# Kernel tuning notes

Hardware: AMD Instinct MI355X
Metric: run time of the kernel (lower is better)

The kernel has to match this reference:

```python
import jax, jax.numpy as jnp
import numpy as np

DIM = 2048
DIM_HEAD = 128
HEADS = 16
BATCH = 1
SEQ = 2048
EPS = 1e-5
MASK_VALUE = 1e-10  # faithful to original module (not -inf)
SCALE = DIM_HEAD ** -0.5


def setup_inputs() -> dict:
    key = jax.random.key(0)
    ks = jax.random.split(key, 7)
    x = jax.random.normal(ks[0], (BATCH, SEQ, DIM), dtype=jnp.float32)
    pos_bias = jax.random.normal(ks[1], (HEADS, SEQ, SEQ), dtype=jnp.float32)
    gamma = jnp.ones((DIM,), dtype=jnp.float32)
    wq = jax.random.normal(ks[2], (DIM, HEADS * DIM_HEAD), dtype=jnp.float32)
    wk = jax.random.normal(ks[3], (DIM, DIM_HEAD), dtype=jnp.float32)
    wv = jax.random.normal(ks[4], (DIM, DIM_HEAD), dtype=jnp.float32)
    wo = jax.random.normal(ks[5], (HEADS * DIM_HEAD, DIM), dtype=jnp.float32)
    # causal mask [SEQ, SEQ]
    mask = jnp.tril(jnp.ones((SEQ, SEQ), dtype=jnp.bool_))
    return {"x": x, "pos_bias": pos_bias, "gamma": gamma,
            "wq": wq, "wk": wk, "wv": wv, "wo": wo, "mask": mask}


def reference(x, pos_bias, gamma, wq, wk, wv, wo, mask):
    # RMSNorm
    inv_norm = jax.lax.rsqrt(jnp.mean(jnp.square(x), axis=-1, keepdims=True) + EPS)
    xn = inv_norm * x * gamma
    # projections (multi-query: single shared K/V head)
    q = xn @ wq                                  # [b, n, h*d]
    k = xn @ wk                                  # [b, n, d]
    v = xn @ wv                                  # [b, n, d]
    b, n, _ = q.shape
    q = q.reshape(b, n, HEADS, DIM_HEAD).transpose(0, 2, 1, 3)  # [b, h, n, d]
    q = q * SCALE
    sim = jnp.einsum('bhid,bjd->bhij', q, k)     # [b, h, i, j]
    sim = sim + pos_bias                          # pos_bias [h, n, n] broadcasts
    sim = jnp.where(mask, sim, MASK_VALUE)
    attn = jax.nn.softmax(sim, axis=-1)
    out = jnp.einsum('bhij,bjd->bhid', attn, v)  # [b, h, n, d]
    out = out.transpose(0, 2, 1, 3).reshape(b, n, HEADS * DIM_HEAD)
    return out @ wo
```

## Files before the change

### kernel.cpp

```cpp
#include <hip/hip_runtime.h>
#include <math.h>

#define SEQ 2048
#define DIM 2048
#define NH 16
#define DH 128
#define NKV 2304
#define KOFF 2048
#define VOFF 2176
#define QK_SCALE 0.08838834764831845f

typedef _Float16 f16;
typedef _Float16 f16x8 __attribute__((ext_vector_type(8)));
typedef _Float16 f16x4 __attribute__((ext_vector_type(4)));
typedef float f32x4 __attribute__((ext_vector_type(4)));

__device__ __forceinline__ void gload16(const f16* g, f16* l) {
    __builtin_amdgcn_global_load_lds(
        (const __attribute__((address_space(1))) void*)g,
        (__attribute__((address_space(3))) void*)l,
        16, 0, 0);
}

__global__ __launch_bounds__(256) void rmsnorm_split_k(
    const float* __restrict__ x, const float* __restrict__ gamma,
    f16* __restrict__ oh, f16* __restrict__ ol)
{
    int row = blockIdx.x, tid = threadIdx.x;
    const float4* xr = (const float4*)(x + (size_t)row * DIM);
    float4 a0 = xr[tid], a1 = xr[tid + 256];
    float ss = a0.x*a0.x + a0.y*a0.y + a0.z*a0.z + a0.w*a0.w
             + a1.x*a1.x + a1.y*a1.y + a1.z*a1.z + a1.w*a1.w;
    #pragma unroll
    for (int off = 1; off < 64; off <<= 1) ss += __shfl_xor(ss, off, 64);
    __shared__ float red[4];
    if ((tid & 63) == 0) red[tid >> 6] = ss;
    __syncthreads();
    float inv = 1.0f / sqrtf((red[0] + red[1] + red[2] + red[3]) * (1.0f / DIM) + 1e-5f);
    const float4* gr = (const float4*)gamma;
    float4 g0 = gr[tid], g1 = gr[tid + 256];
    float v[8] = { a0.x*inv*g0.x, a0.y*inv*g0.y, a0.z*inv*g0.z, a0.w*inv*g0.w,
                   a1.x*inv*g1.x, a1.y*inv*g1.y, a1.z*inv*g1.z, a1.w*inv*g1.w };
    f16x4 h0, l0, h1, l1;
    #pragma unroll
    for (int i = 0; i < 4; i++) {
        f16 h = (f16)v[i];   h0[i] = h; l0[i] = (f16)(v[i]   - (float)h);
        f16 g = (f16)v[i+4]; h1[i] = g; l1[i] = (f16)(v[i+4] - (float)g);
    }
    size_t base = (size_t)row * DIM + tid * 4;
    *(f16x4*)&oh[base] = h0;  *(f16x4*)&oh[base + 1024] = h1;
    *(f16x4*)&ol[base] = l0;  *(f16x4*)&ol[base + 1024] = l1;
}

template<bool WLO>
__global__ __launch_bounds__(256) void transpose_split_k(
    const float* __restrict__ in, f16* __restrict__ oh, f16* __restrict__ ol,
    int ldin, int outld)
{
    __shared__ float t[32][33];
    int tx = threadIdx.x, ty = threadIdx.y;
    int c0 = blockIdx.x * 32, r0 = blockIdx.y * 32;
    #pragma unroll
    for (int yy = 0; yy < 4; yy++)
        t[ty + yy*8][tx] = in[(size_t)(r0 + ty + yy*8) * ldin + c0 + tx];
    __syncthreads();
    #pragma unroll
    for (int yy = 0; yy < 4; yy++) {
        float v = t[tx][ty + yy*8];
        size_t o = (size_t)(c0 + ty + yy*8) * outld + r0 + tx;
        f16 h = (f16)v; oh[o] = h;
        if (WLO) ol[o] = (f16)(v - (float)h);
    }
}

__global__ __launch_bounds__(256) void transpose_f16_k(
    const f16* __restrict__ in, f16* __restrict__ out, int ldin, int outld)
{
    __shared__ f16 t[32][33];
    int tx = threadIdx.x, ty = threadIdx.y;
    int c0 = blockIdx.x * 32, r0 = blockIdx.y * 32;
    #pragma unroll
    for (int yy = 0; yy < 4; yy++)
        t[ty + yy*8][tx] = in[(size_t)(r0 + ty + yy*8) * ldin + c0 + tx];
    __syncthreads();
    #pragma unroll
    for (int yy = 0; yy < 4; yy++)
        out[(size_t)(c0 + ty + yy*8) * outld + r0 + tx] = t[tx][ty + yy*8];
}

__global__ __launch_bounds__(64) void vsuf_k(
    const f16* __restrict__ Vt, float* __restrict__ Vsuf)
{
    int d = blockIdx.x;
    int lane = threadIdx.x;
    float vals[32]; float s = 0.f;
    const f16* row = Vt + (size_t)d * SEQ + lane * 32;
    #pragma unroll
    for (int u = 0; u < 32; u++) { vals[u] = (float)row[u]; s += vals[u]; }
    float acc = s;
    #pragma unroll
    for (int off = 1; off < 64; off <<= 1) {
        float other = __shfl_down(acc, off, 64);
        if (lane + off < 64) acc += other;
    }
    float run = acc - s;
    for (int u = 31; u >= 0; u--) {
        Vsuf[(size_t)(lane * 32 + u) * DH + d] = run;
        run += vals[u];
    }
}

template<int PASSES, int OUTMODE>
__global__ __launch_bounds__(256) void gemm_k(
    const f16* __restrict__ Ah, const f16* __restrict__ Al,
    const f16* __restrict__ Bh, const f16* __restrict__ Bl,
    float* __restrict__ C, f16* __restrict__ Ch, f16* __restrict__ Cl,
    int N, int K, float scale, int scale_cols)
{
    __shared__ f16 sa_h[128 * 32];
    __shared__ f16 sb_h[128 * 32];
    __shared__ f16 sa_l[PASSES == 3 ? 128 * 32 : 8];
    __shared__ f16 sb_l[PASSES == 3 ? 128 * 32 : 8];
    int tid = threadIdx.x;
    int wave = tid >> 6, lane = tid & 63, quad = lane >> 4, l16 = lane & 15;
    int m0 = blockIdx.x * 128, n0 = blockIdx.y * 128;
    int wm = (wave & 1) * 64, wn = (wave >> 1) * 64;
    f32x4 acc[4][4] = {};

    int r0s = wave * 16 + (lane >> 2);
    int cs  = (lane & 3) * 8;
    const f16* gA0 = Ah + (size_t)(m0 + r0s) * K + cs;
    const f16* gA1 = Ah + (size_t)(m0 + r0s + 64) * K + cs;
    const f16* gB0 = Bh + (size_t)(n0 + r0s) * K + cs;
    const f16* gB1 = Bh + (size_t)(n0 + r0s + 64) * K + cs;
    const f16* hA0 = Al + (size_t)(m0 + r0s) * K + cs;
    const f16* hA1 = Al + (size_t)(m0 + r0s + 64) * K + cs;
    const f16* hB0 = Bl + (size_t)(n0 + r0s) * K + cs;
    const f16* hB1 = Bl + (size_t)(n0 + r0s + 64) * K + cs;
    f16* lA0 = &sa_h[(size_t)r0s * 32 + cs];
    f16* lA1 = &sa_h[(size_t)(r0s + 64) * 32 + cs];
    f16* lB0 = &sb_h[(size_t)r0s * 32 + cs];
    f16* lB1 = &sb_h[(size_t)(r0s + 64) * 32 + cs];
    f16* mA0 = &sa_l[(size_t)r0s * 32 + cs];
    f16* mA1 = &sa_l[(size_t)(r0s + 64) * 32 + cs];
    f16* mB0 = &sb_l[(size_t)r0s * 32 + cs];
    f16* mB1 = &sb_l[(size_t)(r0s + 64) * 32 + cs];

    for (int k0 = 0; k0 < K; k0 += 32) {
        __syncthreads();
        gload16(gA0 + k0, lA0);
        gload16(gA1 + k0, lA1);
        gload16(gB0 + k0, lB0);
        gload16(gB1 + k0, lB1);
        if constexpr (PASSES == 3) {
            gload16(hA0 + k0, mA0);
            gload16(hA1 + k0, mA1);
            gload16(hB0 + k0, mB0);
            gload16(hB1 + k0, mB1);
        }
        __syncthreads();
        f16x8 ah[4], bh[4], al[4], bl[4];
        #pragma unroll
        for (int t = 0; t < 4; t++) {
            ah[t] = *(const f16x8*)&sa_h[(wm + t*16 + l16) * 32 + quad * 8];
            bh[t] = *(const f16x8*)&sb_h[(wn + t*16 + l16) * 32 + quad * 8];
        }
        if constexpr (PASSES == 3) {
            #pragma unroll
            for (int t = 0; t < 4; t++) {
                al[t] = *(const f16x8*)&sa_l[(wm + t*16 + l16) * 32 + quad * 8];
                bl[t] = *(const f16x8*)&sb_l[(wn + t*16 + l16) * 32 + quad * 8];
            }
        }
        #pragma unroll
        for (int i = 0; i < 4; i++)
            #pragma unroll
            for (int j = 0; j < 4; j++) {
                acc[i][j] = __builtin_amdgcn_mfma_f32_16x16x32_f16(ah[i], bh[j], acc[i][j], 0, 0, 0);
                if constexpr (PASSES == 3) {
                    acc[i][j] = __builtin_amdgcn_mfma_f32_16x16x32_f16(ah[i], bl[j], acc[i][j], 0, 0, 0);
                    acc[i][j] = __builtin_amdgcn_mfma_f32_16x16x32_f16(al[i], bh[j], acc[i][j], 0, 0, 0);
                }
            }
    }
    #pragma unroll
    for (int i = 0; i < 4; i++)
        #pragma unroll
        for (int j = 0; j < 4; j++) {
            int row = m0 + wm + i*16 + quad*4;
            int col = n0 + wn + j*16 + l16;
            float s = (col < scale_cols) ? scale : 1.0f;
            #pragma unroll
            for (int r = 0; r < 4; r++) {
                float v = acc[i][j][r] * s;
                if constexpr (OUTMODE == 0) {
                    C[(size_t)(row + r) * N + col] = v;
                } else {
                    f16 h = (f16)v;
                    Ch[(size_t)(row + r) * N + col] = h;
                    Cl[(size_t)(row + r) * N + col] = (f16)(v - (float)h);
                }
            }
        }
}

__global__ __launch_bounds__(256) void attn_k(
    const f16* __restrict__ Ph, const f16* __restrict__ Pl,
    const f16* __restrict__ Vt, const float* __restrict__ bias,
    const float* __restrict__ Vsuf, f16* __restrict__ Out)
{
    __shared__ f16 skh[64][136];
    __shared__ f16 skl[64][136];
    __shared__ f16 sv[128][72];
    __shared__ f16 sp[4][16][72];
    int tid = threadIdx.x, wave = tid >> 6, lane = tid & 63;
    int quad = lane >> 4, l16 = lane & 15;
    int h = blockIdx.y;
    int i0 = ((int)gridDim.x - 1 - (int)blockIdx.x) * 64;
    int qrow = i0 + wave * 16 + l16;

    f16x8 qh[4], ql[4];
    #pragma unroll
    for (int kt = 0; kt < 4; kt++) {
        size_t off = (size_t)qrow * NKV + h * DH + kt * 32 + quad * 8;
        qh[kt] = *(const f16x8*)(Ph + off);
        ql[kt] = *(const f16x8*)(Pl + off);
    }
    f32x4 o[8];
    f32x4 zero = {0.f, 0.f, 0.f, 0.f};
    #pragma unroll
    for (int dt = 0; dt < 8; dt++) o[dt] = zero;
    float mrun[4], lrun[4];
    #pragma unroll
    for (int r = 0; r < 4; r++) { mrun[r] = -1e30f; lrun[r] = 0.f; }

    int krow = tid >> 2, kc4 = tid & 3;
    int vd = tid >> 1, vcg = tid & 1;
    const float* brow = bias + (size_t)h * SEQ * SEQ;
    int ibase = i0 + wave * 16 + quad * 4;

    int ntile = i0 / 64 + 1;
    for (int jt = 0; jt < ntile; jt++) {
        int j0 = jt * 64;
        __syncthreads();
        #pragma unroll
        for (int cc = 0; cc < 4; cc++) {
            int ch = kc4 + cc * 4;
            size_t goff = (size_t)(j0 + krow) * NKV + KOFF + ch * 8;
            *(f16x8*)&skh[krow][ch * 8] = *(const f16x8*)(Ph + goff);
            *(f16x8*)&skl[krow][ch * 8] = *(const f16x8*)(Pl + goff);
        }
        #pragma unroll
        for (int cc = 0; cc < 4; cc++) {
            int ch = vcg + cc * 2;
            *(f16x8*)&sv[vd][ch * 8] = *(const f16x8*)(Vt + (size_t)vd * SEQ + j0 + ch * 8);
        }
        __syncthreads();

        f32x4 s[4];
        #pragma unroll
        for (int nt = 0; nt < 4; nt++) s[nt] = zero;
        #pragma unroll
        for (int nt = 0; nt < 4; nt++)
            #pragma unroll
            for (int kt = 0; kt < 4; kt++) {
                f16x8 kh = *(const f16x8*)&skh[nt*16 + l16][kt*32 + quad*8];
                f16x8 kl = *(const f16x8*)&skl[nt*16 + l16][kt*32 + quad*8];
                s[nt] = __builtin_amdgcn_mfma_f32_16x16x32_f16(qh[kt], kh, s[nt], 0, 0, 0);
                s[nt] = __builtin_amdgcn_mfma_f32_16x16x32_f16(qh[kt], kl, s[nt], 0, 0, 0);
                s[nt] = __builtin_amdgcn_mfma_f32_16x16x32_f16(ql[kt], kh, s[nt], 0, 0, 0);
            }
        #pragma unroll
        for (int nt = 0; nt < 4; nt++) {
            int jg = j0 + nt*16 + l16;
            #pragma unroll
            for (int r = 0; r < 4; r++) {
                int ig = ibase + r;
                float v = s[nt][r] + brow[(size_t)ig * SEQ + jg];
                s[nt][r] = (jg <= ig) ? v : 1e-10f;
            }
        }
        #pragma unroll
        for (int r = 0; r < 4; r++) {
            float mx = fmaxf(fmaxf(s[0][r], s[1][r]), fmaxf(s[2][r], s[3][r]));
            mx = fmaxf(mx, __shfl_xor(mx, 1, 64));
            mx = fmaxf(mx, __shfl_xor(mx, 2, 64));
            mx = fmaxf(mx, __shfl_xor(mx, 4, 64));
            mx = fmaxf(mx, __shfl_xor(mx, 8, 64));
            float mn = fmaxf(mrun[r], mx);
            float alpha = __expf(mrun[r] - mn);
            mrun[r] = mn;
            float rs = 0.f;
            #pragma unroll
            for (int nt = 0; nt < 4; nt++) {
                float p = __expf(s[nt][r] - mn);
                s[nt][r] = p; rs += p;
            }
            rs += __shfl_xor(rs, 1, 64);
            rs += __shfl_xor(rs, 2, 64);
            rs += __shfl_xor(rs, 4, 64);
            rs += __shfl_xor(rs, 8, 64);
            lrun[r] = lrun[r] * alpha + rs;
            #pragma unroll
            for (int dt = 0; dt < 8; dt++) o[dt][r] *= alpha;
            #pragma unroll
            for (int nt = 0; nt < 4; nt++)
                sp[wave][quad*4 + r][nt*16 + l16] = (f16)s[nt][r];
        }
        #pragma unroll
        for (int ks = 0; ks < 2; ks++) {
            f16x8 pa = *(const f16x8*)&sp[wave][l16][ks*32 + quad*8];
            #pragma unroll
            for (int dt = 0; dt < 8; dt++) {
                f16x8 vb = *(const f16x8*)&sv[dt*16 + l16][ks*32 + quad*8];
                o[dt] = __builtin_amdgcn_mfma_f32_16x16x32_f16(pa, vb, o[dt], 0, 0, 0);
            }
        }
    }
    #pragma unroll
    for (int dt = 0; dt < 8; dt++) {
        int col = h * DH + dt*16 + l16;
        #pragma unroll
        for (int r = 0; r < 4; r++) {
            int ig = i0 + wave*16 + quad*4 + r;
            int nmask = SEQ - 1 - ig;
            float mfin = fmaxf(mrun[r], 1e-10f);
            float al = __expf(mrun[r] - mfin);
            float pm = (nmask > 0) ? __expf(1e-10f - mfin) : 0.f;
            float lfin = lrun[r] * al + (float)nmask * pm;
            float num = o[dt][r] * al + pm * Vsuf[(size_t)ig * DH + dt*16 + l16];
            Out[(size_t)ig * DIM + col] = (f16)(num / lfin);
        }
    }
}

extern "C" void kernel_launch(void* const* d_in, const int* in_sizes, int n_in,
                              void* d_out, int out_size, void* d_ws, size_t ws_size,
                              hipStream_t stream)
{
    const float* x     = (const float*)d_in[0];
    const float* bias  = (const float*)d_in[1];
    const float* gamma = (const float*)d_in[2];
    const float* wq    = (const float*)d_in[3];
    const float* wk    = (const float*)d_in[4];
    const float* wv    = (const float*)d_in[5];
    const float* wo    = (const float*)d_in[6];
    float* out = (float*)d_out;
    char* ws = (char*)d_ws;

    const size_t MB = 1024 * 1024;
    f16* xn_h   = (f16*)(ws);
    f16* xn_l   = (f16*)(ws + 8  * MB);
    f16* wT_h   = (f16*)(ws + 16 * MB);
    f16* wT_l   = (f16*)(ws + 25 * MB);
    f16* woT_h  = (f16*)(ws + 34 * MB);
    f16* proj_h = (f16*)(ws + 42 * MB);
    f16* proj_l = (f16*)(ws + 51 * MB);
    float* vsuf = (float*)(ws + 60 * MB);
    f16* attn_o = xn_h;
    f16* vT     = xn_l;

    dim3 tb(32, 8);

    rmsnorm_split_k<<<SEQ, 256, 0, stream>>>(x, gamma, xn_h, xn_l);

    transpose_split_k<true><<<dim3(64, 64), tb, 0, stream>>>(wq, wT_h, wT_l, DIM, DIM);
    transpose_split_k<true><<<dim3(4, 64),  tb, 0, stream>>>(wk, wT_h + (size_t)KOFF * DIM,
                                                             wT_l + (size_t)KOFF * DIM, DH, DIM);
    transpose_split_k<true><<<dim3(4, 64),  tb, 0, stream>>>(wv, wT_h + (size_t)VOFF * DIM,
                                                             wT_l + (size_t)VOFF * DIM, DH, DIM);
    transpose_split_k<false><<<dim3(64, 64), tb, 0, stream>>>(wo, woT_h, nullptr, DIM, DIM);

    gemm_k<3, 1><<<dim3(16, 18), 256, 0, stream>>>(xn_h, xn_l, wT_h, wT_l,
                                                   nullptr, proj_h, proj_l,
                                                   NKV, DIM, QK_SCALE, DIM);

    transpose_f16_k<<<dim3(4, 64), tb, 0, stream>>>(proj_h + VOFF, vT, NKV, SEQ);
    vsuf_k<<<DH, 64, 0, stream>>>(vT, vsuf);

    attn_k<<<dim3(32, 16), 256, 0, stream>>>(proj_h, proj_l, vT, bias, vsuf, attn_o);

    gemm_k<1, 0><<<dim3(16, 16), 256, 0, stream>>>(attn_o, attn_o, woT_h, woT_h,
                                                   out, nullptr, nullptr,
                                                   DIM, DIM, 1.0f, 0);
}
```

Baseline: 783.1 us.

## Split causal attention rows into KV halves with atomic work queue and merge

The attention kernel becomes persistent: each block pulls work units from an atomic counter, longest-first. Each query-row tile of 64 rows is split into two halves of its causal KV range. The partial outputs, row max and row sum are written to a workspace buffer, and a separate merge kernel combines them with the masked-suffix correction. The aim is to balance the triangular causal workload across CUs. The cost is partial writes, an extra merge launch, a counter-reset launch, and rounding the normalized partials to fp16.

Result: faster. 680.1 us (-13.2%).

```diff
diff --git a/kernel.cpp b/kernel.cpp
--- a/kernel.cpp
+++ b/kernel.cpp
@@ -9,6 +9,9 @@
 #define KOFF 2048
 #define VOFF 2176
 #define QK_SCALE 0.08838834764831845f
+
+#define NUNITS 1008
+#define RECS 16896
 
 typedef _Float16 f16;
 typedef _Float16 f16x8 __attribute__((ext_vector_type(8)));
@@ -109,6 +112,8 @@
         run += vals[u];
     }
 }
+
+__global__ void init_counter_k(int* c) { c[0] = 0; }
 
 template<int PASSES, int OUTMODE>
 __global__ __launch_bounds__(256) void gemm_k(
@@ -207,130 +212,217 @@
 __global__ __launch_bounds__(256) void attn_k(
     const f16* __restrict__ Ph, const f16* __restrict__ Pl,
     const f16* __restrict__ Vt, const float* __restrict__ bias,
-    const float* __restrict__ Vsuf, f16* __restrict__ Out)
+    const float* __restrict__ Vsuf, f16* __restrict__ Out,
+    char* __restrict__ partial, int* __restrict__ counter)
 {
     __shared__ f16 skh[64][136];
     __shared__ f16 skl[64][136];
     __shared__ f16 sv[128][72];
     __shared__ f16 sp[4][16][72];
+    __shared__ int s_unit;
     int tid = threadIdx.x, wave = tid >> 6, lane = tid & 63;
     int quad = lane >> 4, l16 = lane & 15;
-    int h = blockIdx.y;
-    int i0 = ((int)gridDim.x - 1 - (int)blockIdx.x) * 64;
-    int qrow = i0 + wave * 16 + l16;
-
-    f16x8 qh[4], ql[4];
-    #pragma unroll
-    for (int kt = 0; kt < 4; kt++) {
-        size_t off = (size_t)qrow * NKV + h * DH + kt * 32 + quad * 8;
-        qh[kt] = *(const f16x8*)(Ph + off);
-        ql[kt] = *(const f16x8*)(Pl + off);
-    }
-    f32x4 o[8];
-    f32x4 zero = {0.f, 0.f, 0.f, 0.f};
-    #pragma unroll
-    for (int dt = 0; dt < 8; dt++) o[dt] = zero;
-    float mrun[4], lrun[4];
-    #pragma unroll
-    for (int r = 0; r < 4; r++) { mrun[r] = -1e30f; lrun[r] = 0.f; }
-
     int krow = tid >> 2, kc4 = tid & 3;
     int vd = tid >> 1, vcg = tid & 1;
-    const float* brow = bias + (size_t)h * SEQ * SEQ;
-    int ibase = i0 + wave * 16 + quad * 4;
-
-    int ntile = i0 / 64 + 1;
-    for (int jt = 0; jt < ntile; jt++) {
-        int j0 = jt * 64;
+    f32x4 zero = {0.f, 0.f, 0.f, 0.f};
+
+    for (;;) {
         __syncthreads();
-        #pragma unroll
-        for (int cc = 0; cc < 4; cc++) {
-            int ch = kc4 + cc * 4;
-            size_t goff = (size_t)(j0 + krow) * NKV + KOFF + ch * 8;
-            *(f16x8*)&skh[krow][ch * 8] = *(const f16x8*)(Ph + goff);
-            *(f16x8*)&skl[krow][ch * 8] = *(const f16x8*)(Pl + goff);
-        }
-        #pragma unroll
-        for (int cc = 0; cc < 4; cc++) {
-            int ch = vcg + cc * 2;
-            *(f16x8*)&sv[vd][ch * 8] = *(const f16x8*)(Vt + (size_t)vd * SEQ + j0 + ch * 8);
-        }
+        if (tid == 0) s_unit = atomicAdd(counter, 1);
         __syncthreads();
-
-        f32x4 s[4];
-        #pragma unroll
-        for (int nt = 0; nt < 4; nt++) s[nt] = zero;
-        #pragma unroll
-        for (int nt = 0; nt < 4; nt++)
-            #pragma unroll
-            for (int kt = 0; kt < 4; kt++) {
-                f16x8 kh = *(const f16x8*)&skh[nt*16 + l16][kt*32 + quad*8];
-                f16x8 kl = *(const f16x8*)&skl[nt*16 + l16][kt*32 + quad*8];
-                s[nt] = __builtin_amdgcn_mfma_f32_16x16x32_f16(qh[kt], kh, s[nt], 0, 0, 0);
-                s[nt] = __builtin_amdgcn_mfma_f32_16x16x32_f16(qh[kt], kl, s[nt], 0, 0, 0);
-                s[nt] = __builtin_amdgcn_mfma_f32_16x16x32_f16(ql[kt], kh, s[nt], 0, 0, 0);
-            }
-        #pragma unroll
-        for (int nt = 0; nt < 4; nt++) {
-            int jg = j0 + nt*16 + l16;
+        int u = s_unit;
+        if (u >= NUNITS) break;
+
+        int a, h, jt_begin, jt_end, is_half;
+        if (u < 992) {
+            int pr = u >> 5; a = 31 - pr; h = u & 15;
+            int half = (u >> 4) & 1;
+            int ntt = a + 1, nth = (ntt + 1) >> 1;
+            jt_begin = half ? nth : 0;
+            jt_end   = half ? ntt : nth;
+            is_half = 1;
+        } else {
+            a = 0; h = u - 992; jt_begin = 0; jt_end = 1; is_half = 0;
+        }
+        int i0 = a * 64;
+        int qrow = i0 + wave * 16 + l16;
+        int ibase = i0 + wave * 16 + quad * 4;
+        const float* brow = bias + (size_t)h * SEQ * SEQ;
+
+        f16x8 qh[4], ql[4];
+        #pragma unroll
+        for (int kt = 0; kt < 4; kt++) {
+            size_t off = (size_t)qrow * NKV + h * DH + kt * 32 + quad * 8;
+            qh[kt] = *(const f16x8*)(Ph + off);
+            ql[kt] = *(const f16x8*)(Pl + off);
+        }
+        f32x4 o[8];
+        #pragma unroll
+        for (int dt = 0; dt < 8; dt++) o[dt] = zero;
+        float mrun[4], lrun[4];
+        #pragma unroll
+        for (int r = 0; r < 4; r++) { mrun[r] = -1e30f; lrun[r] = 0.f; }
+
+        for (int jt = jt_begin; jt < jt_end; jt++) {
+            int j0 = jt * 64;
+            __syncthreads();
+            #pragma unroll
+            for (int cc = 0; cc < 4; cc++) {
+                int ch = kc4 + cc * 4;
+                size_t goff = (size_t)(j0 + krow) * NKV + KOFF + ch * 8;
+                *(f16x8*)&skh[krow][ch * 8] = *(const f16x8*)(Ph + goff);
+                *(f16x8*)&skl[krow][ch * 8] = *(const f16x8*)(Pl + goff);
+            }
+            #pragma unroll
+            for (int cc = 0; cc < 4; cc++) {
+                int ch = vcg + cc * 2;
+                *(f16x8*)&sv[vd][ch * 8] = *(const f16x8*)(Vt + (size_t)vd * SEQ + j0 + ch * 8);
+            }
+            __syncthreads();
+
+            f32x4 s[4];
+            #pragma unroll
+            for (int nt = 0; nt < 4; nt++) s[nt] = zero;
+            #pragma unroll
+            for (int nt = 0; nt < 4; nt++)
+                #pragma unroll
+                for (int kt = 0; kt < 4; kt++) {
+                    f16x8 kh = *(const f16x8*)&skh[nt*16 + l16][kt*32 + quad*8];
+                    f16x8 kl = *(const f16x8*)&skl[nt*16 + l16][kt*32 + quad*8];
+                    s[nt] = __builtin_amdgcn_mfma_f32_16x16x32_f16(qh[kt], kh, s[nt], 0, 0, 0);
+                    s[nt] = __builtin_amdgcn_mfma_f32_16x16x32_f16(qh[kt], kl, s[nt], 0, 0, 0);
+                    s[nt] = __builtin_amdgcn_mfma_f32_16x16x32_f16(ql[kt], kh, s[nt], 0, 0, 0);
+                }
+            #pragma unroll
+            for (int nt = 0; nt < 4; nt++) {
+                int jg = j0 + nt*16 + l16;
+                #pragma unroll
+                for (int r = 0; r < 4; r++) {
+                    int ig = ibase + r;
+                    float v = s[nt][r] + brow[(size_t)ig * SEQ + jg];
+                    s[nt][r] = (jg <= ig) ? v : 1e-10f;
+                }
+            }
             #pragma unroll
             for (int r = 0; r < 4; r++) {
-                int ig = ibase + r;
-                float v = s[nt][r] + brow[(size_t)ig * SEQ + jg];
-                s[nt][r] = (jg <= ig) ? v : 1e-10f;
-            }
-        }
-        #pragma unroll
-        for (int r = 0; r < 4; r++) {
-            float mx = fmaxf(fmaxf(s[0][r], s[1][r]), fmaxf(s[2][r], s[3][r]));
-            mx = fmaxf(mx, __shfl_xor(mx, 1, 64));
-            mx = fmaxf(mx, __shfl_xor(mx, 2, 64));
-            mx = fmaxf(mx, __shfl_xor(mx, 4, 64));
-            mx = fmaxf(mx, __shfl_xor(mx, 8, 64));
-            float mn = fmaxf(mrun[r], mx);
-            float alpha = __expf(mrun[r] - mn);
-            mrun[r] = mn;
-            float rs = 0.f;
-            #pragma unroll
-            for (int nt = 0; nt < 4; nt++) {
-                float p = __expf(s[nt][r] - mn);
-                s[nt][r] = p; rs += p;
-            }
-            rs += __shfl_xor(rs, 1, 64);
-            rs += __shfl_xor(rs, 2, 64);
-            rs += __shfl_xor(rs, 4, 64);
-            rs += __shfl_xor(rs, 8, 64);
-            lrun[r] = lrun[r] * alpha + rs;
-            #pragma unroll
-            for (int dt = 0; dt < 8; dt++) o[dt][r] *= alpha;
-            #pragma unroll
-            for (int nt = 0; nt < 4; nt++)
-                sp[wave][quad*4 + r][nt*16 + l16] = (f16)s[nt][r];
-        }
-        #pragma unroll
-        for (int ks = 0; ks < 2; ks++) {
-            f16x8 pa = *(const f16x8*)&sp[wave][l16][ks*32 + quad*8];
+                float mx = fmaxf(fmaxf(s[0][r], s[1][r]), fmaxf(s[2][r], s[3][r]));
+                mx = fmaxf(mx, __shfl_xor(mx, 1, 64));
+                mx = fmaxf(mx, __shfl_xor(mx, 2, 64));
+                mx = fmaxf(mx, __shfl_xor(mx, 4, 64));
+                mx = fmaxf(mx, __shfl_xor(mx, 8, 64));
+                float mn = fmaxf(mrun[r], mx);
+                float alpha = __expf(mrun[r] - mn);
+                mrun[r] = mn;
+                float rs = 0.f;
+                #pragma unroll
+                for (int nt = 0; nt < 4; nt++) {
+                    float p = __expf(s[nt][r] - mn);
+                    s[nt][r] = p; rs += p;
+                }
+                rs += __shfl_xor(rs, 1, 64);
+                rs += __shfl_xor(rs, 2, 64);
+                rs += __shfl_xor(rs, 4, 64);
+                rs += __shfl_xor(rs, 8, 64);
+                lrun[r] = lrun[r] * alpha + rs;
+                #pragma unroll
+                for (int dt = 0; dt < 8; dt++) o[dt][r] *= alpha;
+                #pragma unroll
+                for (int nt = 0; nt < 4; nt++)
+                    sp[wave][quad*4 + r][nt*16 + l16] = (f16)s[nt][r];
+            }
+            #pragma unroll
+            for (int ks = 0; ks < 2; ks++) {
+                f16x8 pa = *(const f16x8*)&sp[wave][l16][ks*32 + quad*8];
+                #pragma unroll
+                for (int dt = 0; dt < 8; dt++) {
+                    f16x8 vb = *(const f16x8*)&sv[dt*16 + l16][ks*32 + quad*8];
+                    o[dt] = __builtin_amdgcn_mfma_f32_16x16x32_f16(pa, vb, o[dt], 0, 0, 0);
+                }
+            }
+        }
+
+        if (is_half) {
+            char* rec = partial + (size_t)u * RECS;
+            f16*   on = (f16*)rec;
+            float* pm = (float*)(rec + 16384);
+            float* pl = (float*)(rec + 16640);
+            float invl[4];
+            #pragma unroll
+            for (int r = 0; r < 4; r++) invl[r] = 1.0f / lrun[r];
+            #pragma unroll
+            for (int dt = 0; dt < 8; dt++)
+                #pragma unroll
+                for (int r = 0; r < 4; r++)
+                    on[(wave*16 + quad*4 + r) * DH + dt*16 + l16] = (f16)(o[dt][r] * invl[r]);
+            if (l16 == 0) {
+                #pragma unroll
+                for (int r = 0; r < 4; r++) {
+                    int row = wave*16 + quad*4 + r;
+                    pm[row] = mrun[r]; pl[row] = lrun[r];
+                }
+            }
+        } else {
             #pragma unroll
             for (int dt = 0; dt < 8; dt++) {
-                f16x8 vb = *(const f16x8*)&sv[dt*16 + l16][ks*32 + quad*8];
-                o[dt] = __builtin_amdgcn_mfma_f32_16x16x32_f16(pa, vb, o[dt], 0, 0, 0);
-            }
-        }
-    }
-    #pragma unroll
-    for (int dt = 0; dt < 8; dt++) {
-        int col = h * DH + dt*16 + l16;
-        #pragma unroll
-        for (int r = 0; r < 4; r++) {
-            int ig = i0 + wave*16 + quad*4 + r;
-            int nmask = SEQ - 1 - ig;
-            float mfin = fmaxf(mrun[r], 1e-10f);
-            float al = __expf(mrun[r] - mfin);
-            float pm = (nmask > 0) ? __expf(1e-10f - mfin) : 0.f;
-            float lfin = lrun[r] * al + (float)nmask * pm;
-            float num = o[dt][r] * al + pm * Vsuf[(size_t)ig * DH + dt*16 + l16];
-            Out[(size_t)ig * DIM + col] = (f16)(num / lfin);
-        }
+                int col = h * DH + dt*16 + l16;
+                #pragma unroll
+                for (int r = 0; r < 4; r++) {
+                    int ig = i0 + wave*16 + quad*4 + r;
+                    int nmask = SEQ - 1 - ig;
+                    float mfin = fmaxf(mrun[r], 1e-10f);
+                    float al = __expf(mrun[r] - mfin);
+                    float pmv = (nmask > 0) ? __expf(1e-10f - mfin) : 0.f;
+                    float lfin = lrun[r] * al + (float)nmask * pmv;
+                    float num = o[dt][r] * al + pmv * Vsuf[(size_t)ig * DH + dt*16 + l16];
+                    Out[(size_t)ig * DIM + col] = (f16)(num / lfin);
+                }
+            }
+        }
+    }
+}
+
+__global__ __launch_bounds__(256) void attn_merge_k(
+    const char* __restrict__ partial, const float* __restrict__ Vsuf,
+    f16* __restrict__ Out)
+{
+    int b = blockIdx.x;
+    int pr = b >> 4, h = b & 15;
+    int a = 31 - pr, i0 = a * 64;
+    int u0 = pr * 32 + h, u1 = u0 + 16;
+    const char* r0 = partial + (size_t)u0 * RECS;
+    const char* r1 = partial + (size_t)u1 * RECS;
+    const f16*   o1p = (const f16*)r0;
+    const float* m1p = (const float*)(r0 + 16384);
+    const float* l1p = (const float*)(r0 + 16640);
+    const f16*   o2p = (const f16*)r1;
+    const float* m2p = (const float*)(r1 + 16384);
+    const float* l2p = (const float*)(r1 + 16640);
+    int t = threadIdx.x;
+    int col = (t & 15) * 8;
+    int rg = t >> 4;
+    #pragma unroll
+    for (int rr = 0; rr < 4; rr++) {
+        int row = rg * 4 + rr, ig = i0 + row;
+        float m1 = m1p[row], l1 = l1p[row], m2 = m2p[row], l2 = l2p[row];
+        float m = fmaxf(m1, m2);
+        float w1 = __expf(m1 - m) * l1;
+        float w2 = __expf(m2 - m) * l2;
+        float l = w1 + w2;
+        int nmask = SEQ - 1 - ig;
+        float mf = fmaxf(m, 1e-10f);
+        float al = __expf(m - mf);
+        float pm = (nmask > 0) ? __expf(1e-10f - mf) : 0.f;
+        float lf = l * al + (float)nmask * pm;
+        f16x8 o1 = *(const f16x8*)&o1p[row * DH + col];
+        f16x8 o2 = *(const f16x8*)&o2p[row * DH + col];
+        const float* vs = &Vsuf[(size_t)ig * DH + col];
+        f16x8 outv;
+        #pragma unroll
+        for (int e = 0; e < 8; e++) {
+            float num = ((float)o1[e] * w1 + (float)o2[e] * w2) * al + pm * vs[e];
+            outv[e] = (f16)(num / lf);
+        }
+        *(f16x8*)&Out[(size_t)ig * DIM + h * DH + col] = outv;
     }
 }
 
@@ -357,6 +449,8 @@
     f16* proj_h = (f16*)(ws + 42 * MB);
     f16* proj_l = (f16*)(ws + 51 * MB);
     float* vsuf = (float*)(ws + 60 * MB);
+    char* partial = ws + 16 * MB;
+    int* counter  = (int*)(ws + 33 * MB);
     f16* attn_o = xn_h;
     f16* vT     = xn_l;
 
@@ -377,8 +471,11 @@
 
     transpose_f16_k<<<dim3(4, 64), tb, 0, stream>>>(proj_h + VOFF, vT, NKV, SEQ);
     vsuf_k<<<DH, 64, 0, stream>>>(vT, vsuf);
-
-    attn_k<<<dim3(32, 16), 256, 0, stream>>>(proj_h, proj_l, vT, bias, vsuf, attn_o);
+    init_counter_k<<<1, 1, 0, stream>>>(counter);
+
+    attn_k<<<512, 256, 0, stream>>>(proj_h, proj_l, vT, bias, vsuf, attn_o,
+                                    partial, counter);
+    attn_merge_k<<<496, 256, 0, stream>>>(partial, vsuf, attn_o);
 
     gemm_k<1, 0><<<dim3(16, 16), 256, 0, stream>>>(attn_o, attn_o, woT_h, woT_h,
                                                    out, nullptr, nullptr,
```

## Split-KV persistent attention with atomic work queue, async bias prefetch, and merge pass

Applied to the files above, without the earlier changes.

Replaces the per-block causal attention kernel with a persistent kernel that pulls work units from an atomic counter. Each unit is one 16-row query group and head, with long rows split into up to four KV chunks so that work is balanced across the causal triangle. Each wave reads K and V straight from global memory, prefetches pos_bias into double-buffered LDS using global_load_lds with an XOR swizzle, and writes normalized partial outputs plus max and sum statistics. A separate merge kernel then combines the partials and adds the masked-suffix correction, which now uses a per-64-column-chunk V sum table. This adds a counter reset launch, a merge launch and partial-buffer traffic, and drops the LDS reuse of K/V across waves.

Measured after the change: 741.2 us. -5.4%, faster.

```diff
diff --git a/kernel.cpp b/kernel.cpp
--- a/kernel.cpp
+++ b/kernel.cpp
@@ -10,12 +10,22 @@
 #define VOFF 2176
 #define QK_SCALE 0.08838834764831845f
 
+#define NUNITS2 5120
+#define RECB 4224
+#define RECPH 288
+
 typedef _Float16 f16;
 typedef _Float16 f16x8 __attribute__((ext_vector_type(8)));
 typedef _Float16 f16x4 __attribute__((ext_vector_type(4)));
 typedef float f32x4 __attribute__((ext_vector_type(4)));
 
 __device__ __forceinline__ void gload16(const f16* g, f16* l) {
+    __builtin_amdgcn_global_load_lds(
+        (const __attribute__((address_space(1))) void*)g,
+        (__attribute__((address_space(3))) void*)l,
+        16, 0, 0);
+}
+__device__ __forceinline__ void gload16f(const float* g, float* l) {
     __builtin_amdgcn_global_load_lds(
         (const __attribute__((address_space(1))) void*)g,
         (__attribute__((address_space(3))) void*)l,
@@ -88,27 +98,25 @@
         out[(size_t)(c0 + ty + yy*8) * outld + r0 + tx] = t[tx][ty + yy*8];
 }
 
-__global__ __launch_bounds__(64) void vsuf_k(
-    const f16* __restrict__ Vt, float* __restrict__ Vsuf)
-{
-    int d = blockIdx.x;
-    int lane = threadIdx.x;
-    float vals[32]; float s = 0.f;
-    const f16* row = Vt + (size_t)d * SEQ + lane * 32;
-    #pragma unroll
-    for (int u = 0; u < 32; u++) { vals[u] = (float)row[u]; s += vals[u]; }
-    float acc = s;
+__global__ __launch_bounds__(64) void vsuft_k(
+    const f16* __restrict__ Vt, float* __restrict__ Vsuft)
+{
+    int d = blockIdx.x, t = threadIdx.x;
+    float s = 0.f;
+    if (t < 32) {
+        const f16* row = Vt + (size_t)d * SEQ + t * 64;
+        #pragma unroll
+        for (int u = 0; u < 64; u++) s += (float)row[u];
+    }
     #pragma unroll
     for (int off = 1; off < 64; off <<= 1) {
-        float other = __shfl_down(acc, off, 64);
-        if (lane + off < 64) acc += other;
-    }
-    float run = acc - s;
-    for (int u = 31; u >= 0; u--) {
-        Vsuf[(size_t)(lane * 32 + u) * DH + d] = run;
-        run += vals[u];
-    }
-}
+        float v = __shfl_down(s, off, 64);
+        s += (t + off < 64) ? v : 0.f;
+    }
+    if (t <= 32) Vsuft[t * DH + d] = (t < 32) ? s : 0.f;
+}
+
+__global__ void init_counter_k(int* c) { c[0] = 0; }
 
 template<int PASSES, int OUTMODE>
 __global__ __launch_bounds__(256) void gemm_k(
@@ -204,133 +212,230 @@
         }
 }
 
-__global__ __launch_bounds__(256) void attn_k(
+__global__ __launch_bounds__(256) void attn2_k(
     const f16* __restrict__ Ph, const f16* __restrict__ Pl,
     const f16* __restrict__ Vt, const float* __restrict__ bias,
-    const float* __restrict__ Vsuf, f16* __restrict__ Out)
-{
-    __shared__ f16 skh[64][136];
-    __shared__ f16 skl[64][136];
-    __shared__ f16 sv[128][72];
-    __shared__ f16 sp[4][16][72];
+    const float* __restrict__ Vsuft, f16* __restrict__ Out,
+    char* __restrict__ partial, int* __restrict__ counter)
+{
+    __shared__ float sbias[4 * 2 * 1024];
+    __shared__ f16 sp[4 * 16 * 72];
     int tid = threadIdx.x, wave = tid >> 6, lane = tid & 63;
     int quad = lane >> 4, l16 = lane & 15;
-    int h = blockIdx.y;
-    int i0 = ((int)gridDim.x - 1 - (int)blockIdx.x) * 64;
-    int qrow = i0 + wave * 16 + l16;
-
-    f16x8 qh[4], ql[4];
-    #pragma unroll
-    for (int kt = 0; kt < 4; kt++) {
-        size_t off = (size_t)qrow * NKV + h * DH + kt * 32 + quad * 8;
-        qh[kt] = *(const f16x8*)(Ph + off);
-        ql[kt] = *(const f16x8*)(Pl + off);
-    }
-    f32x4 o[8];
+    float* mybias = &sbias[wave * 2048];
+    f16* mysp = &sp[wave * 1152];
+    int dma_r = lane >> 4;
+    int dma_c = lane & 15;
     f32x4 zero = {0.f, 0.f, 0.f, 0.f};
-    #pragma unroll
-    for (int dt = 0; dt < 8; dt++) o[dt] = zero;
-    float mrun[4], lrun[4];
-    #pragma unroll
-    for (int r = 0; r < 4; r++) { mrun[r] = -1e30f; lrun[r] = 0.f; }
-
-    int krow = tid >> 2, kc4 = tid & 3;
-    int vd = tid >> 1, vcg = tid & 1;
-    const float* brow = bias + (size_t)h * SEQ * SEQ;
-    int ibase = i0 + wave * 16 + quad * 4;
-
-    int ntile = i0 / 64 + 1;
-    for (int jt = 0; jt < ntile; jt++) {
-        int j0 = jt * 64;
-        __syncthreads();
-        #pragma unroll
-        for (int cc = 0; cc < 4; cc++) {
-            int ch = kc4 + cc * 4;
-            size_t goff = (size_t)(j0 + krow) * NKV + KOFF + ch * 8;
-            *(f16x8*)&skh[krow][ch * 8] = *(const f16x8*)(Ph + goff);
-            *(f16x8*)&skl[krow][ch * 8] = *(const f16x8*)(Pl + goff);
-        }
-        #pragma unroll
-        for (int cc = 0; cc < 4; cc++) {
-            int ch = vcg + cc * 2;
-            *(f16x8*)&sv[vd][ch * 8] = *(const f16x8*)(Vt + (size_t)vd * SEQ + j0 + ch * 8);
-        }
-        __syncthreads();
-
-        f32x4 s[4];
-        #pragma unroll
-        for (int nt = 0; nt < 4; nt++) s[nt] = zero;
-        #pragma unroll
-        for (int nt = 0; nt < 4; nt++)
-            #pragma unroll
-            for (int kt = 0; kt < 4; kt++) {
-                f16x8 kh = *(const f16x8*)&skh[nt*16 + l16][kt*32 + quad*8];
-                f16x8 kl = *(const f16x8*)&skl[nt*16 + l16][kt*32 + quad*8];
-                s[nt] = __builtin_amdgcn_mfma_f32_16x16x32_f16(qh[kt], kh, s[nt], 0, 0, 0);
-                s[nt] = __builtin_amdgcn_mfma_f32_16x16x32_f16(qh[kt], kl, s[nt], 0, 0, 0);
-                s[nt] = __builtin_amdgcn_mfma_f32_16x16x32_f16(ql[kt], kh, s[nt], 0, 0, 0);
-            }
-        #pragma unroll
-        for (int nt = 0; nt < 4; nt++) {
-            int jg = j0 + nt*16 + l16;
-            #pragma unroll
-            for (int r = 0; r < 4; r++) {
-                int ig = ibase + r;
-                float v = s[nt][r] + brow[(size_t)ig * SEQ + jg];
-                s[nt][r] = (jg <= ig) ? v : 1e-10f;
-            }
-        }
-        #pragma unroll
-        for (int r = 0; r < 4; r++) {
-            float mx = fmaxf(fmaxf(s[0][r], s[1][r]), fmaxf(s[2][r], s[3][r]));
-            mx = fmaxf(mx, __shfl_xor(mx, 1, 64));
-            mx = fmaxf(mx, __shfl_xor(mx, 2, 64));
-            mx = fmaxf(mx, __shfl_xor(mx, 4, 64));
-            mx = fmaxf(mx, __shfl_xor(mx, 8, 64));
-            float mn = fmaxf(mrun[r], mx);
-            float alpha = __expf(mrun[r] - mn);
-            mrun[r] = mn;
+
+    for (;;) {
+        int u0;
+        if (lane == 0) u0 = atomicAdd(counter, 1);
+        int u = __shfl(u0, 0, 64);
+        if (u >= NUNITS2) break;
+
+        int h = u & 15, t = u >> 4;
+        int g, chunk, n;
+        if (t < 128)      { g = 127 - (t >> 2); chunk = t & 3; n = 4; }
+        else if (t < 224) { int s5 = t - 128; int q5 = s5 / 3; g = 95 - q5; chunk = s5 - q5 * 3; n = 3; }
+        else if (t < 288) { int s5 = t - 224; g = 63 - (s5 >> 1); chunk = s5 & 1; n = 2; }
+        else              { g = 31 - (t - 288); chunk = 0; n = 1; }
+        int c = (g >> 2) + 1;
+        int bse = c / n, rem = c % n;
+        int jt0 = chunk * bse + (chunk < rem ? chunk : rem);
+        int jt1 = jt0 + bse + (chunk < rem ? 1 : 0);
+        int ig = g * 16 + l16;
+        const float* bgh = bias + (size_t)h * SEQ * SEQ + (size_t)(g * 16) * SEQ;
+
+        f16x8 qh[4], ql[4];
+        #pragma unroll
+        for (int kt = 0; kt < 4; kt++) {
+            size_t off = (size_t)ig * NKV + h * DH + kt * 32 + quad * 8;
+            qh[kt] = *(const f16x8*)(Ph + off);
+            ql[kt] = *(const f16x8*)(Pl + off);
+        }
+        f32x4 o[8];
+        #pragma unroll
+        for (int dt = 0; dt < 8; dt++) o[dt] = zero;
+        float mrun = -1e30f, lrun = 0.f;
+
+        {
+            int j0 = jt0 * 64;
+            #pragma unroll
+            for (int qq = 0; qq < 4; qq++) {
+                int rl = qq * 4 + dma_r;
+                const float* src = bgh + (size_t)rl * SEQ + j0 + ((dma_c ^ rl) << 2);
+                gload16f(src, mybias + qq * 256);
+            }
+        }
+
+        int bi = 0;
+        for (int jt = jt0; jt < jt1; jt++, bi ^= 1) {
+            int j0 = jt * 64;
+            f32x4 s[4];
+            #pragma unroll
+            for (int nt = 0; nt < 4; nt++) {
+                const f16* kb = Ph + (size_t)(j0 + nt * 16 + l16) * NKV + KOFF + quad * 8;
+                const f16* lb = Pl + (size_t)(j0 + nt * 16 + l16) * NKV + KOFF + quad * 8;
+                f16x8 kh[4], kl[4];
+                #pragma unroll
+                for (int kt = 0; kt < 4; kt++) {
+                    kh[kt] = *(const f16x8*)(kb + kt * 32);
+                    kl[kt] = *(const f16x8*)(lb + kt * 32);
+                }
+                s[nt] = zero;
+                #pragma unroll
+                for (int kt = 0; kt < 4; kt++) {
+                    s[nt] = __builtin_amdgcn_mfma_f32_16x16x32_f16(kh[kt], qh[kt], s[nt], 0, 0, 0);
+                    s[nt] = __builtin_amdgcn_mfma_f32_16x16x32_f16(kl[kt], qh[kt], s[nt], 0, 0, 0);
+                    s[nt] = __builtin_amdgcn_mfma_f32_16x16x32_f16(kh[kt], ql[kt], s[nt], 0, 0, 0);
+                }
+            }
+            __builtin_amdgcn_s_waitcnt(0x0F70);
+            const float* bb = mybias + bi * 1024;
+            #pragma unroll
+            for (int nt = 0; nt < 4; nt++) {
+                f32x4 bv = *(const f32x4*)&bb[(l16 << 6) + (((nt * 4 + quad) ^ l16) << 2)];
+                #pragma unroll
+                for (int r = 0; r < 4; r++) {
+                    int jg = j0 + nt * 16 + quad * 4 + r;
+                    s[nt][r] = (jg <= ig) ? (s[nt][r] + bv[r]) : 1e-10f;
+                }
+            }
+            float mx = -1e30f;
+            #pragma unroll
+            for (int nt = 0; nt < 4; nt++)
+                #pragma unroll
+                for (int r = 0; r < 4; r++) mx = fmaxf(mx, s[nt][r]);
+            mx = fmaxf(mx, __shfl_xor(mx, 16, 64));
+            mx = fmaxf(mx, __shfl_xor(mx, 32, 64));
+            float mn = fmaxf(mrun, mx);
+            float alpha = __expf(mrun - mn);
+            mrun = mn;
             float rs = 0.f;
             #pragma unroll
             for (int nt = 0; nt < 4; nt++) {
-                float p = __expf(s[nt][r] - mn);
-                s[nt][r] = p; rs += p;
-            }
-            rs += __shfl_xor(rs, 1, 64);
-            rs += __shfl_xor(rs, 2, 64);
-            rs += __shfl_xor(rs, 4, 64);
-            rs += __shfl_xor(rs, 8, 64);
-            lrun[r] = lrun[r] * alpha + rs;
-            #pragma unroll
-            for (int dt = 0; dt < 8; dt++) o[dt][r] *= alpha;
-            #pragma unroll
-            for (int nt = 0; nt < 4; nt++)
-                sp[wave][quad*4 + r][nt*16 + l16] = (f16)s[nt][r];
-        }
-        #pragma unroll
-        for (int ks = 0; ks < 2; ks++) {
-            f16x8 pa = *(const f16x8*)&sp[wave][l16][ks*32 + quad*8];
+                f16x4 pv;
+                #pragma unroll
+                for (int r = 0; r < 4; r++) {
+                    float p = __expf(s[nt][r] - mn);
+                    rs += p; pv[r] = (f16)p;
+                }
+                *(f16x4*)&mysp[l16 * 72 + nt * 16 + quad * 4] = pv;
+            }
+            rs += __shfl_xor(rs, 16, 64);
+            rs += __shfl_xor(rs, 32, 64);
+            lrun = lrun * alpha + rs;
+            #pragma unroll
+            for (int dt = 0; dt < 8; dt++) o[dt] *= alpha;
+            #pragma unroll
+            for (int ks = 0; ks < 2; ks++) {
+                f16x8 pa = *(const f16x8*)&mysp[l16 * 72 + ks * 32 + quad * 8];
+                #pragma unroll
+                for (int dt = 0; dt < 8; dt++) {
+                    f16x8 va = *(const f16x8*)(Vt + (size_t)(dt * 16 + l16) * SEQ + j0 + ks * 32 + quad * 8);
+                    o[dt] = __builtin_amdgcn_mfma_f32_16x16x32_f16(va, pa, o[dt], 0, 0, 0);
+                }
+            }
+            if (jt + 1 < jt1) {
+                int j0n = (jt + 1) * 64;
+                #pragma unroll
+                for (int qq = 0; qq < 4; qq++) {
+                    int rl = qq * 4 + dma_r;
+                    const float* src = bgh + (size_t)rl * SEQ + j0n + ((dma_c ^ rl) << 2);
+                    gload16f(src, mybias + (bi ^ 1) * 1024 + qq * 256);
+                }
+            }
+        }
+
+        if (n == 1) {
+            int nm = SEQ - 64 * c;
+            float mf = fmaxf(mrun, 1e-10f);
+            float al = __expf(mrun - mf);
+            float pm = (nm > 0) ? __expf(1e-10f - mf) : 0.f;
+            float lf = lrun * al + (float)nm * pm;
+            float inv = 1.0f / lf;
             #pragma unroll
             for (int dt = 0; dt < 8; dt++) {
-                f16x8 vb = *(const f16x8*)&sv[dt*16 + l16][ks*32 + quad*8];
-                o[dt] = __builtin_amdgcn_mfma_f32_16x16x32_f16(pa, vb, o[dt], 0, 0, 0);
-            }
-        }
-    }
-    #pragma unroll
-    for (int dt = 0; dt < 8; dt++) {
-        int col = h * DH + dt*16 + l16;
-        #pragma unroll
-        for (int r = 0; r < 4; r++) {
-            int ig = i0 + wave*16 + quad*4 + r;
-            int nmask = SEQ - 1 - ig;
-            float mfin = fmaxf(mrun[r], 1e-10f);
-            float al = __expf(mrun[r] - mfin);
-            float pm = (nmask > 0) ? __expf(1e-10f - mfin) : 0.f;
-            float lfin = lrun[r] * al + (float)nmask * pm;
-            float num = o[dt][r] * al + pm * Vsuf[(size_t)ig * DH + dt*16 + l16];
-            Out[(size_t)ig * DIM + col] = (f16)(num / lfin);
-        }
+                f32x4 vs = *(const f32x4*)&Vsuft[c * DH + dt * 16 + quad * 4];
+                f16x4 ov;
+                #pragma unroll
+                for (int r = 0; r < 4; r++)
+                    ov[r] = (f16)((o[dt][r] * al + pm * vs[r]) * inv);
+                *(f16x4*)&Out[(size_t)ig * DIM + h * DH + dt * 16 + quad * 4] = ov;
+            }
+        } else {
+            int cg = (g < 64) ? (g - 32) * 2 : (g < 96) ? 64 + (g - 64) * 3 : 160 + (g - 96) * 4;
+            char* rec = partial + ((size_t)h * RECPH + cg + chunk) * RECB;
+            f16* on = (f16*)rec;
+            float inv = 1.0f / lrun;
+            #pragma unroll
+            for (int dt = 0; dt < 8; dt++) {
+                f16x4 ov;
+                #pragma unroll
+                for (int r = 0; r < 4; r++) ov[r] = (f16)(o[dt][r] * inv);
+                *(f16x4*)&on[l16 * DH + dt * 16 + quad * 4] = ov;
+            }
+            if (quad == 0) {
+                *(float*)(rec + 4096 + l16 * 4) = mrun;
+                *(float*)(rec + 4160 + l16 * 4) = lrun;
+            }
+        }
+    }
+}
+
+__global__ __launch_bounds__(64) void attn_merge2_k(
+    const char* __restrict__ partial, const float* __restrict__ Vsuft,
+    f16* __restrict__ Out)
+{
+    int b = blockIdx.x;
+    int g = 32 + (b >> 4), h = b & 15;
+    int n = (g >> 5) + 1;
+    int c = (g >> 2) + 1;
+    int t = threadIdx.x;
+    int row = t >> 2, cq = t & 3;
+    int cg = (g < 64) ? (g - 32) * 2 : (g < 96) ? 64 + (g - 64) * 3 : 160 + (g - 96) * 4;
+    const char* rec0 = partial + ((size_t)h * RECPH + cg) * RECB;
+
+    float mk[4], lk[4], w[4];
+    float ms = -1e30f;
+    for (int k = 0; k < n; k++) {
+        const char* r = rec0 + (size_t)k * RECB;
+        mk[k] = *(const float*)(r + 4096 + row * 4);
+        lk[k] = *(const float*)(r + 4160 + row * 4);
+        ms = fmaxf(ms, mk[k]);
+    }
+    float L = 0.f;
+    for (int k = 0; k < n; k++) { w[k] = __expf(mk[k] - ms) * lk[k]; L += w[k]; }
+
+    float acc[32];
+    #pragma unroll
+    for (int e = 0; e < 32; e++) acc[e] = 0.f;
+    for (int k = 0; k < n; k++) {
+        const f16* ov = (const f16*)(rec0 + (size_t)k * RECB) + row * DH + cq * 32;
+        #pragma unroll
+        for (int e = 0; e < 4; e++) {
+            f16x8 v = *(const f16x8*)(ov + e * 8);
+            #pragma unroll
+            for (int uu = 0; uu < 8; uu++) acc[e * 8 + uu] += w[k] * (float)v[uu];
+        }
+    }
+    int ig = g * 16 + row;
+    int nm = SEQ - 64 * c;
+    float mf = fmaxf(ms, 1e-10f);
+    float al = __expf(ms - mf);
+    float pm = (nm > 0) ? __expf(1e-10f - mf) : 0.f;
+    float lf = L * al + (float)nm * pm;
+    float inv = 1.0f / lf;
+    const float* vs = Vsuft + c * DH + cq * 32;
+    f16* op = Out + (size_t)ig * DIM + h * DH + cq * 32;
+    #pragma unroll
+    for (int e = 0; e < 4; e++) {
+        f16x8 ov;
+        #pragma unroll
+        for (int uu = 0; uu < 8; uu++)
+            ov[uu] = (f16)((acc[e * 8 + uu] * al + pm * vs[e * 8 + uu]) * inv);
+        *(f16x8*)(op + e * 8) = ov;
     }
 }
 
@@ -353,12 +458,14 @@
     f16* xn_l   = (f16*)(ws + 8  * MB);
     f16* wT_h   = (f16*)(ws + 16 * MB);
     f16* wT_l   = (f16*)(ws + 25 * MB);
-    f16* woT_h  = (f16*)(ws + 34 * MB);
-    f16* proj_h = (f16*)(ws + 42 * MB);
-    f16* proj_l = (f16*)(ws + 51 * MB);
-    float* vsuf = (float*)(ws + 60 * MB);
+    char* partial = ws + 16 * MB;
+    f16* woT_h  = (f16*)(ws + 36 * MB);
+    f16* proj_h = (f16*)(ws + 44 * MB);
+    f16* proj_l = (f16*)(ws + 53 * MB);
     f16* attn_o = xn_h;
-    f16* vT     = xn_l;
+    f16* vT     = (f16*)(ws + 8 * MB);
+    float* vsuft = (float*)(ws + 8 * MB + 512 * 1024);
+    int* counter = (int*)(ws + 9 * MB);
 
     dim3 tb(32, 8);
 
@@ -376,9 +483,12 @@
                                                    NKV, DIM, QK_SCALE, DIM);
 
     transpose_f16_k<<<dim3(4, 64), tb, 0, stream>>>(proj_h + VOFF, vT, NKV, SEQ);
-    vsuf_k<<<DH, 64, 0, stream>>>(vT, vsuf);
-
-    attn_k<<<dim3(32, 16), 256, 0, stream>>>(proj_h, proj_l, vT, bias, vsuf, attn_o);
+    vsuft_k<<<DH, 64, 0, stream>>>(vT, vsuft);
+    init_counter_k<<<1, 1, 0, stream>>>(counter);
+
+    attn2_k<<<768, 256, 0, stream>>>(proj_h, proj_l, vT, bias, vsuft, attn_o,
+                                     partial, counter);
+    attn_merge2_k<<<1536, 64, 0, stream>>>(partial, vsuft, attn_o);
 
     gemm_k<1, 0><<<dim3(16, 16), 256, 0, stream>>>(attn_o, attn_o, woT_h, woT_h,
                                                    out, nullptr, nullptr,
```
